# Optimization experiments

Measured on AMD Instinct MI355X. Metric: run time of the kernel, lower is better.

## Reference

```python
import jax, jax.numpy as jnp
import numpy as np

TAU = 1.0
BASE = 7
NUM_TWISTS = 3
EPS = 1e-6

B, S, D, P, M = 4, 2048, 1024, 9, 256


def _rot(y, theta):
    # learned rotation in the (0,1) channel plane; theta broadcasts against y[..., 0]
    c, s = jnp.cos(theta), jnp.sin(theta)
    y0, y1 = y[..., 0], y[..., 1]
    r0 = (y0 * c - y1 * s)[..., None]
    r1 = (y0 * s + y1 * c)[..., None]
    return jnp.concatenate([r0, r1, y[..., 2:]], axis=-1)


def _mod_phase_norm(x, g, base=BASE):
    # RMS-normalize within channel groups defined by (channel index mod base)
    d = x.shape[-1]
    gid = jnp.arange(d) % base
    oh = jax.nn.one_hot(gid, base, dtype=x.dtype)           # [d, base]
    cnt = oh.sum(axis=0)                                    # [base]
    msq = (x * x) @ oh / cnt                                # [..., base]
    denom = jnp.sqrt(jnp.take(msq, gid, axis=-1) + EPS)     # [..., d]
    return x / denom * g


def setup_inputs() -> dict:
    key = jax.random.key(0)
    ks = jax.random.split(key, 16)
    w = lambda k, shape, scale: jax.random.normal(k, shape, dtype=jnp.float32) * scale
    u = jax.random.uniform(ks[1], (NUM_TWISTS + 1, B, S, P), dtype=jnp.float32,
                           minval=1e-6, maxval=1.0 - 1e-6)
    gumbel_noise = -jnp.log(-jnp.log(u))
    return {
        'x': w(ks[0], (B, S, D), 1.0),
        'gumbel_noise': gumbel_noise,
        'mixer_w': w(ks[2], (3, D), 0.5),
        'obs_W1': w(ks[3], (2 * D, M), (2 * D) ** -0.5),
        'obs_b1': jnp.zeros((M,), jnp.float32),
        'obs_th1': w(ks[4], (), 0.1),
        'obs_W2': w(ks[5], (M, P), M ** -0.5),
        'obs_b2': jnp.zeros((P,), jnp.float32),
        'obs_th2': w(ks[6], (), 0.1),
        'path_Wa': w(ks[7], (P, D, M), D ** -0.5),
        'path_ba': jnp.zeros((P, M), jnp.float32),
        'path_tha': w(ks[8], (P,), 0.1),
        'path_Wb': w(ks[9], (P, M, D), M ** -0.5),
        'path_bb': jnp.zeros((P, D), jnp.float32),
        'path_thb': w(ks[10], (P,), 0.1),
        'twist_W': w(ks[11], (D, D), D ** -0.5),
        'twist_b': jnp.zeros((D,), jnp.float32),
        'twist_th': w(ks[12], (), 0.1),
        'norm_g': jnp.ones((D,), jnp.float32),
    }


def reference(x, gumbel_noise, mixer_w, obs_W1, obs_b1, obs_th1, obs_W2, obs_b2,
              obs_th2, path_Wa, path_ba, path_tha, path_Wb, path_bb, path_thb,
              twist_W, twist_b, twist_th, norm_g):
    # neighbor mixer: per-channel 3-tap mix over sequence (zero-padded, non-causal)
    xp = jnp.pad(x, ((0, 0), (1, 1), (0, 0)))
    x_mixed = x * mixer_w[0] + xp[:, :-2] * mixer_w[1] + xp[:, 2:] * mixer_w[2]

    def observer_logits(collapsed):
        combined = jnp.concatenate([x_mixed, collapsed], axis=-1)      # [B,S,2D]
        h = jnp.tanh(_rot(combined @ obs_W1 + obs_b1, obs_th1))        # [B,S,M]
        return _rot(h @ obs_W2 + obs_b2, obs_th2)                      # [B,S,P]

    def path_outputs_fn(tin):
        h = _rot(jnp.einsum('bsd,pdm->bspm', tin, path_Wa) + path_ba, path_tha)
        return _rot(jnp.einsum('bspm,pmd->bspd', h, path_Wb) + path_bb, path_thb)

    collapsed = jnp.zeros_like(x_mixed)
    path_out = None
    for t in range(NUM_TWISTS):
        logits = observer_logits(collapsed)
        rw = jax.nn.softmax((logits + gumbel_noise[t]) / TAU, axis=-1)  # soft gumbel
        tin = x_mixed + _rot(collapsed @ twist_W + twist_b, twist_th)
        path_out = path_outputs_fn(tin)                                # [B,S,P,D]
        collapsed = _mod_phase_norm(jnp.einsum('bspd,bsp->bsd', path_out, rw), norm_g)

    # final hard (straight-through) gumbel routing, reusing last path_out
    final_logits = observer_logits(collapsed)
    soft = jax.nn.softmax((final_logits + gumbel_noise[NUM_TWISTS]) / TAU, axis=-1)
    hard = jax.nn.one_hot(jnp.argmax(soft, axis=-1), P, dtype=soft.dtype)
    rw_hard = hard + soft - jax.lax.stop_gradient(soft)
    final_collapsed = jnp.einsum('bspd,bsp->bsd', path_out, rw_hard)

    # dropout is identity in eval mode
    out = _mod_phase_norm(x + final_collapsed, norm_g)
    collapsed = _mod_phase_norm(collapsed, norm_g)
    return out, collapsed
```

## Files before the change

### kernel.cpp

```cpp
#include <hip/hip_runtime.h>
#include <hip/hip_bf16.h>

typedef unsigned short u16;
typedef short bf16x8 __attribute__((ext_vector_type(8)));
typedef float f32x4 __attribute__((ext_vector_type(4)));

constexpr int Dd = 1024, Pp = 9, Mm = 256, Nn = 8192, Kc = 2304;
constexpr float EPSf = 1e-6f;

__device__ __forceinline__ float bf2f(u16 u) {
    union { unsigned int u; float f; } v; v.u = ((unsigned int)u) << 16; return v.f;
}
__device__ __forceinline__ u16 f2bf(float f) {
    union { float f; unsigned int u; } v; v.f = f;
    unsigned int r = (v.u + 0x7FFFu + ((v.u >> 16) & 1u)) >> 16; return (u16)r;
}
__device__ __forceinline__ void split2(float v, u16& h, u16& l) {
    h = f2bf(v); l = f2bf(v - bf2f(h));
}
__device__ __forceinline__ void gld16(u16* lds, const u16* g) {
    __builtin_amdgcn_global_load_lds(
        (const __attribute__((address_space(1))) unsigned int*)g,
        (__attribute__((address_space(3))) unsigned int*)lds, 16, 0, 0);
}
// ... 18 lines not shown
}

__global__ void splitW1_k(const float* __restrict__ W1, const float* __restrict__ th,
                          u16* __restrict__ h, u16* __restrict__ l)
{
    int idx = blockIdx.x * 256 + threadIdx.x;
    if (idx >= 256 * 2048) return;
    int k = idx & 2047, n = idx >> 11;
    float v;
    if (n == 0)      v = W1[(long)k * 256 + 0] * cosf(th[0]) - W1[(long)k * 256 + 1] * sinf(th[0]);
    else if (n == 1) v = W1[(long)k * 256 + 0] * sinf(th[0]) + W1[(long)k * 256 + 1] * cosf(th[0]);
    else             v = W1[(long)k * 256 + n];
    u16 hh, ll; split2(v, hh, ll); h[idx] = hh; l[idx] = ll;
}

__global__ void splitTW_k(const float* __restrict__ tW, const float* __restrict__ th,
                          u16* __restrict__ h, u16* __restrict__ l)
{
    int idx = blockIdx.x * 256 + threadIdx.x;
    if (idx >= 1024 * 1024) return;
    int k = idx & 1023, n = idx >> 10;
    float v;
    if (n == 0)      v = tW[(long)k * 1024 + 0] * cosf(th[0]) - tW[(long)k * 1024 + 1] * sinf(th[0]);
    else if (n == 1) v = tW[(long)k * 1024 + 0] * sinf(th[0]) + tW[(long)k * 1024 + 1] * cosf(th[0]);
    else             v = tW[(long)k * 1024 + n];
    u16 hh, ll; split2(v, hh, ll); h[idx] = hh; l[idx] = ll;
}

__global__ void splitWa_k(const float* __restrict__ Wa, const float* __restrict__ tha,
                          u16* __restrict__ h, u16* __restrict__ l)
{
    int idx = blockIdx.x * 256 + threadIdx.x;
    if (idx >= Kc * 1024) return;
    int k = idx & 1023, n = idx >> 10;
    int p = n >> 8, m = n & 255;
    const float* s = Wa + ((long)p * 1024 + k) * 256;
    float v;
    if (m == 0)      v = s[0] * cosf(tha[p]) - s[1] * sinf(tha[p]);
    else if (m == 1) v = s[0] * sinf(tha[p]) + s[1] * cosf(tha[p]);
    else             v = s[m];
// ... 2 lines not shown

__global__ void splitWb_k(const float* __restrict__ Wb, const float* __restrict__ thb,
                          u16* __restrict__ h, u16* __restrict__ l)
{
    int idx = blockIdx.x * 256 + threadIdx.x;
    if (idx >= 1024 * Kc) return;
    int n = idx / Kc;
    int k = idx - n * Kc;
    int p = k >> 8, m = k & 255;
    const float* s = Wb + ((long)p * 256 + m) * 1024;
    float v;
    if (n == 0)      v = s[0] * cosf(thb[p]) - s[1] * sinf(thb[p]);
    else if (n == 1) v = s[0] * sinf(thb[p]) + s[1] * cosf(thb[p]);
    else             v = s[n];
    u16 hh, ll; split2(v, hh, ll); h[idx] = hh; l[idx] = ll;
}

__global__ void mixer_k(const float* __restrict__ x, const float* __restrict__ mw,
                        u16* __restrict__ xmh, u16* __restrict__ xml)
{
    int idx = blockIdx.x * 256 + threadIdx.x;
    if (idx >= Nn * Dd / 4) return;
    int d4 = idx & (Dd / 4 - 1);
    int n = idx >> 8;
    int s = n & 2047;
    const float4* x4 = (const float4*)x;
    const float4* w4 = (const float4*)mw;
    float4 xc = x4[idx];
    float4 w0 = w4[d4], w1 = w4[(Dd / 4) + d4], w2 = w4[2 * (Dd / 4) + d4];
    float o[4];
// ... 6 lines not shown
        float4 xr = x4[idx + Dd / 4];
        o[0] += xr.x * w2.x; o[1] += xr.y * w2.y; o[2] += xr.z * w2.z; o[3] += xr.w * w2.w;
    }
    ushort4 h4, l4;
    split2(o[0], h4.x, l4.x); split2(o[1], h4.y, l4.y);
    split2(o[2], h4.z, l4.z); split2(o[3], h4.w, l4.w);
    ((ushort4*)xmh)[idx] = h4; ((ushort4*)xml)[idx] = l4;
}

__global__ void tanh_k(const float* __restrict__ a, float* __restrict__ o, int total)
{
    int idx = blockIdx.x * 256 + threadIdx.x;
    if (idx < total) o[idx] = tanhf(a[idx]);
}

__global__ void addb_split_k(const u16* __restrict__ xmh, const u16* __restrict__ xml,
                             const float* __restrict__ tbr,
                             u16* __restrict__ th_, u16* __restrict__ tl_)
{
    int idx = blockIdx.x * 256 + threadIdx.x;
    if (idx >= Nn * Dd / 4) return;
    int d4 = idx & (Dd / 4 - 1);
    ushort4 xh = ((const ushort4*)xmh)[idx], xl = ((const ushort4*)xml)[idx];
    float4 b = ((const float4*)tbr)[d4];
    ushort4 h4, l4;
    split2(bf2f(xh.x) + bf2f(xl.x) + b.x, h4.x, l4.x);
    split2(bf2f(xh.y) + bf2f(xl.y) + b.y, h4.y, l4.y);
    split2(bf2f(xh.z) + bf2f(xl.z) + b.z, h4.z, l4.z);
    split2(bf2f(xh.w) + bf2f(xl.w) + b.w, h4.w, l4.w);
    ((ushort4*)th_)[idx] = h4; ((ushort4*)tl_)[idx] = l4;
}

template<int EPI>
__global__ __launch_bounds__(256, 2) void mgemm(
    const u16* __restrict__ Agh, const u16* __restrict__ Agl, int lda,
    const u16* __restrict__ Bgh, const u16* __restrict__ Bgl, int ldb,
    int K,
    float* __restrict__ Cf, int ldc,
    const float* __restrict__ Cinit,
    const float* __restrict__ bias,
    const float* __restrict__ rwv,
    const float* __restrict__ rwv2,
    const float* __restrict__ bbrv)
{
    __shared__ u16 smem[2][16384];
    const int tid = threadIdx.x, wave = tid >> 6, lane = tid & 63;
    const int nwg = gridDim.x * gridDim.y;
    const int flat = blockIdx.y * gridDim.x + blockIdx.x;
    const int q = nwg >> 3;
    const int l_ = (flat & 7) * q + (flat >> 3);
    const int r0 = (l_ / gridDim.x) * 128, c0 = (l_ % gridDim.x) * 128;
    const int srl = lane >> 2;
    const int ssl = ((lane & 3) ^ ((lane >> 3) & 3)) * 8;
    const int frl = lane & 15, kh = lane >> 4;
    const int sw  = (kh ^ ((frl >> 1) & 3)) * 8;
    const int arow0 = (wave >> 1) * 64, bcol0 = (wave & 1) * 64;
    const int w32 = wave * 32;

    f32x4 acc[4][4] = {};
    f32x4 acc2[4][4];
    if constexpr (EPI == 4) {
#pragma unroll
        for (int i = 0; i < 4; ++i)
#pragma unroll
            for (int j = 0; j < 4; ++j) acc2[i][j] = f32x4{0.f, 0.f, 0.f, 0.f};
    }

    auto STAGE = [&](int buf, int k0) {
        u16* base = &smem[buf][0];
        u16* As_h = base;        u16* As_l = base + 4096;
        u16* Bs_h = base + 8192; u16* Bs_l = base + 12288;
        const long ga0 = (long)(r0 + w32 + srl) * lda + k0 + ssl;
        gld16(&As_h[w32 * 32],        Agh + ga0);
        gld16(&As_h[(w32 + 16) * 32], Agh + ga0 + 16L * lda);
        gld16(&As_l[w32 * 32],        Agl + ga0);
        gld16(&As_l[(w32 + 16) * 32], Agl + ga0 + 16L * lda);
        const long gb0 = (long)(c0 + w32 + srl) * ldb + k0 + ssl;
        gld16(&Bs_h[w32 * 32],        Bgh + gb0);
        gld16(&Bs_h[(w32 + 16) * 32], Bgh + gb0 + 16L * ldb);
        gld16(&Bs_l[w32 * 32],        Bgl + gb0);
        gld16(&Bs_l[(w32 + 16) * 32], Bgl + gb0 + 16L * ldb);
    };
    auto COMPUTE = [&](int buf, f32x4 (&ac)[4][4]) {
        u16* base = &smem[buf][0];
        u16* As_h = base;        u16* As_l = base + 4096;
        u16* Bs_h = base + 8192; u16* Bs_l = base + 12288;
        bf16x8 ah[4], al[4];
#pragma unroll
        for (int f = 0; f < 4; ++f) {
            int ao = (arow0 + f * 16 + frl) * 32 + sw;
            ah[f] = *(const bf16x8*)&As_h[ao];
            al[f] = *(const bf16x8*)&As_l[ao];
        }
#pragma unroll
        for (int j = 0; j < 4; ++j) {
            int bo = (bcol0 + j * 16 + frl) * 32 + sw;
            bf16x8 bh = *(const bf16x8*)&Bs_h[bo];
            bf16x8 bl = *(const bf16x8*)&Bs_l[bo];
#pragma unroll
            for (int i = 0; i < 4; ++i) {
                ac[i][j] = __builtin_amdgcn_mfma_f32_16x16x32_bf16(ah[i], bh, ac[i][j], 0, 0, 0);
                ac[i][j] = __builtin_amdgcn_mfma_f32_16x16x32_bf16(ah[i], bl, ac[i][j], 0, 0, 0);
                ac[i][j] = __builtin_amdgcn_mfma_f32_16x16x32_bf16(al[i], bh, ac[i][j], 0, 0, 0);
            }
        }
    };
    auto FLUSH = [&](int p) {
#pragma unroll
        for (int i = 0; i < 4; ++i)
#pragma unroll
            for (int reg = 0; reg < 4; ++reg) {
                float w = rwv[(long)(r0 + arow0 + i * 16 + kh * 4 + reg) * 9 + p];
#pragma unroll
                for (int j = 0; j < 4; ++j) {
                    acc[i][j][reg] += w * acc2[i][j][reg];
                    acc2[i][j][reg] = 0.f;
                }
            }
    };

    const int NT = K / 32;
    STAGE(0, 0);
#pragma unroll 1
    for (int t = 0; t < NT; t += 2) {
        STAGE(1, (t + 1) * 32);
        asm volatile("s_waitcnt vmcnt(8)" ::: "memory");
        __builtin_amdgcn_sched_barrier(0);
        __builtin_amdgcn_s_barrier();
        __builtin_amdgcn_sched_barrier(0);
        if constexpr (EPI == 4) COMPUTE(0, acc2); else COMPUTE(0, acc);
        __builtin_amdgcn_sched_barrier(0);
        __builtin_amdgcn_s_barrier();
        __builtin_amdgcn_sched_barrier(0);
        if (t + 2 < NT) {
            STAGE(0, (t + 2) * 32);
            asm volatile("s_waitcnt vmcnt(8)" ::: "memory");
        } else {
            asm volatile("s_waitcnt vmcnt(0)" ::: "memory");
        }
        __builtin_amdgcn_sched_barrier(0);
        __builtin_amdgcn_s_barrier();
        __builtin_amdgcn_sched_barrier(0);
        if constexpr (EPI == 4) COMPUTE(1, acc2); else COMPUTE(1, acc);
        __builtin_amdgcn_sched_barrier(0);
        __builtin_amdgcn_s_barrier();
        __builtin_amdgcn_sched_barrier(0);
        if constexpr (EPI == 4) {
            if (((t + 1) & 7) == 7) FLUSH((t + 1) >> 3);
        }
    }

#pragma unroll
    for (int i = 0; i < 4; ++i)
#pragma unroll
        for (int reg = 0; reg < 4; ++reg) {
            const int r = r0 + arow0 + i * 16 + kh * 4 + reg;
#pragma unroll
            for (int j = 0; j < 4; ++j) {
                const int c = c0 + bcol0 + j * 16 + frl;
                float v = acc[i][j][reg];
                if constexpr (EPI == 0) {
                    Cf[(long)r * ldc + c] = v + bias[c];
                } else if constexpr (EPI == 1) {
                    Cf[(long)r * ldc + c] = tanhf(v + Cinit[(long)r * ldc + c]);
                } else if constexpr (EPI == 4) {
#pragma unroll
                    for (int p = 0; p < 9; ++p) v += rwv2[(long)r * 9 + p] * bbrv[p * 1024 + c];
                    Cf[(long)r * ldc + c] = v;
                }
            }
        }
}

template<int EPI>
__global__ __launch_bounds__(512, 2) void mgemm3(
    const u16* __restrict__ Agh, const u16* __restrict__ Agl, int lda,
    const u16* __restrict__ Bgh, const u16* __restrict__ Bgl, int ldb,
    int K,
    float* __restrict__ Cf, u16* __restrict__ Coh, u16* __restrict__ Col, int ldc,
    const u16* __restrict__ CIh, const u16* __restrict__ CIl,
    const float* __restrict__ bias,
    const float* __restrict__ rwv,
    const float* __restrict__ bbrv)
{
    __shared__ u16 smem[2][24576];
    const int tid = threadIdx.x, wave = tid >> 6, lane = tid & 63;
    const int nwg = gridDim.x * gridDim.y;
    const int flat = blockIdx.y * gridDim.x + blockIdx.x;
    const int q = nwg >> 3;
    const int l_ = (flat & 7) * q + (flat >> 3);
    const int r0 = (l_ / gridDim.x) * 256, c0 = (l_ % gridDim.x) * 128;
    const int srl = lane >> 2;
    const int ssl = ((lane & 3) ^ ((lane >> 3) & 3)) * 8;
    const int frl = lane & 15, kh = lane >> 4;
    const int sw  = (kh ^ ((frl >> 1) & 3)) * 8;
    const int arow0 = (wave >> 1) * 64, bcol0 = (wave & 1) * 64;
    const int w32 = wave * 32, w16 = wave * 16;
    const int NT = K / 32;

    f32x4 acc[4][4] = {};

    auto STAGE = [&](int buf, int k0) {
        u16* Ash = &smem[buf][0];
        u16* Asl = &smem[buf][8192];
        u16* Bsh = &smem[buf][16384];
        u16* Bsl = &smem[buf][20480];
        const long ga = (long)(r0 + w32 + srl) * lda + k0 + ssl;
        gld16(&Ash[w32 * 32],        Agh + ga);
        gld16(&Ash[(w32 + 16) * 32], Agh + ga + 16L * lda);
        gld16(&Asl[w32 * 32],        Agl + ga);
        gld16(&Asl[(w32 + 16) * 32], Agl + ga + 16L * lda);
        const long gb = (long)(c0 + w16 + srl) * ldb + k0 + ssl;
        gld16(&Bsh[w16 * 32], Bgh + gb);
        gld16(&Bsl[w16 * 32], Bgl + gb);
    };
    auto COMPUTE = [&](int buf) {
        const u16* Ash = &smem[buf][0];
        const u16* Asl = &smem[buf][8192];
        const u16* Bsh = &smem[buf][16384];
        const u16* Bsl = &smem[buf][20480];
        bf16x8 ah[4], al[4], bh[4], bl[4];
#pragma unroll
        for (int f = 0; f < 4; ++f) {
            int ao = (arow0 + f * 16 + frl) * 32 + sw;
            ah[f] = *(const bf16x8*)&Ash[ao];
            al[f] = *(const bf16x8*)&Asl[ao];
            int bo = (bcol0 + f * 16 + frl) * 32 + sw;
            bh[f] = *(const bf16x8*)&Bsh[bo];
            bl[f] = *(const bf16x8*)&Bsl[bo];
        }
        __builtin_amdgcn_s_setprio(1);
#pragma unroll
        for (int j = 0; j < 4; ++j)
#pragma unroll
            for (int i = 0; i < 4; ++i) {
                acc[i][j] = __builtin_amdgcn_mfma_f32_16x16x32_bf16(ah[i], bh[j], acc[i][j], 0, 0, 0);
                acc[i][j] = __builtin_amdgcn_mfma_f32_16x16x32_bf16(ah[i], bl[j], acc[i][j], 0, 0, 0);
                acc[i][j] = __builtin_amdgcn_mfma_f32_16x16x32_bf16(al[i], bh[j], acc[i][j], 0, 0, 0);
            }
        __builtin_amdgcn_s_setprio(0);
    };

    STAGE(0, 0);
    asm volatile("s_waitcnt vmcnt(0)" ::: "memory");
    __builtin_amdgcn_sched_barrier(0);
    __builtin_amdgcn_s_barrier();
    __builtin_amdgcn_sched_barrier(0);

#pragma unroll 1
    for (int t = 0; t < NT; t += 2) {
        STAGE(1, (t + 1) * 32);
        COMPUTE(0);
        asm volatile("s_waitcnt vmcnt(0)" ::: "memory");
        __builtin_amdgcn_sched_barrier(0);
        __builtin_amdgcn_s_barrier();
        __builtin_amdgcn_sched_barrier(0);
        if (t + 2 < NT) STAGE(0, (t + 2) * 32);
        COMPUTE(1);
        asm volatile("s_waitcnt vmcnt(0)" ::: "memory");
        __builtin_amdgcn_sched_barrier(0);
        __builtin_amdgcn_s_barrier();
        __builtin_amdgcn_sched_barrier(0);
    }

#pragma unroll
    for (int i = 0; i < 4; ++i)
#pragma unroll
        for (int reg = 0; reg < 4; ++reg) {
            const int r = r0 + arow0 + i * 16 + kh * 4 + reg;
#pragma unroll
            for (int j = 0; j < 4; ++j) {
                const int c = c0 + bcol0 + j * 16 + frl;
                float v = acc[i][j][reg];
                if constexpr (EPI == 2) {
                    long o = (long)r * ldc + c;
                    v += bf2f(CIh[o]) + bf2f(CIl[o]) + bias[c];
                    u16 h, l; split2(v, h, l); Coh[o] = h; Col[o] = l;
                } else if constexpr (EPI == 3) {
                    long o = (long)r * ldc + c;
                    v = (v + bias[c]) * rwv[(long)r * 9 + (c >> 8)];
                    u16 h, l; split2(v, h, l); Coh[o] = h; Col[o] = l;
                } else {
#pragma unroll
                    for (int p = 0; p < 9; ++p) v += rwv[(long)r * 9 + p] * bbrv[p * 1024 + c];
                    Cf[(long)r * ldc + c] = v;
                }
            }
        }
}

__global__ void logits_k(const float* __restrict__ h, const float* __restrict__ W2r,
                         const float* __restrict__ b2r, const float* __restrict__ gum,
                         float* __restrict__ rwA, float* __restrict__ rwH,
                         const float* __restrict__ rwS, int hard)
{
    __shared__ float hs[Mm];
    __shared__ float lg[16];
    int n = blockIdx.x;
    for (int i = threadIdx.x; i < Mm; i += 64) hs[i] = h[(long)n * Mm + i];
    __syncthreads();
    if (threadIdx.x < Pp) {
        int p = threadIdx.x;
        float acc = b2r[p];
        for (int m = 0; m < Mm; ++m) acc += hs[m] * W2r[m * Pp + p];
        lg[p] = acc + gum[(long)n * Pp + p];
    }
    __syncthreads();
    if (threadIdx.x == 0) {
        float mx = lg[0]; int am = 0;
#pragma unroll
        for (int p = 1; p < Pp; ++p) if (lg[p] > mx) { mx = lg[p]; am = p; }
        if (hard) {
#pragma unroll
            for (int p = 0; p < Pp; ++p) {
                rwA[(long)n * Pp + p] = (p == am) ? 1.f / rwS[(long)n * Pp + p] : 0.f;
                rwH[(long)n * Pp + p] = (p == am) ? 1.f : 0.f;
            }
        } else {
            float e[Pp]; float ssum = 0.f;
#pragma unroll
            for (int p = 0; p < Pp; ++p) { e[p] = expf(lg[p] - mx); ssum += e[p]; }
#pragma unroll
            for (int p = 0; p < Pp; ++p) rwA[(long)n * Pp + p] = e[p] / ssum;
        }
    }
}

template<int INSPLIT, int OUTSPLIT>
__global__ void norm_k(const float* __restrict__ in,
                       const u16* __restrict__ inh, const u16* __restrict__ inl,
                       const float* __restrict__ add, const float* __restrict__ g,
                       float* __restrict__ outf, u16* __restrict__ oh, u16* __restrict__ ol)
// ... 26 lines not shown
        const float cnt = (t < 2) ? 147.f : 146.f;
        dn[t] = 1.f / sqrtf(sb[0][t] / cnt + EPSf);
    }
    __syncthreads();
#pragma unroll
    for (int i = 0; i < 4; ++i) {
        int d = t + i * 256;
        long o = (long)n * Dd + d;
        float ov = v[i] * dn[d % 7] * g[d];
        if (OUTSPLIT) { u16 h, l; split2(ov, h, l); oh[o] = h; ol[o] = l; }
        else outf[o] = ov;
    }
}

static inline int cdiv(long a, long b) { return (int)((a + b - 1) / b); }

extern "C" void kernel_launch(void* const* d_in, const int* in_sizes, int n_in,
                              void* d_out, int out_size, void* d_ws, size_t ws_size,
                              hipStream_t stream)
{
    const float* x    = (const float*)d_in[0];
    const float* gum  = (const float*)d_in[1];
    const float* mw   = (const float*)d_in[2];
    const float* W1   = (const float*)d_in[3];
    const float* b1   = (const float*)d_in[4];
    const float* th1  = (const float*)d_in[5];
    const float* W2   = (const float*)d_in[6];
    const float* b2   = (const float*)d_in[7];
    const float* th2  = (const float*)d_in[8];
    const float* Wa   = (const float*)d_in[9];
    const float* ba   = (const float*)d_in[10];
    const float* tha  = (const float*)d_in[11];
    const float* Wb   = (const float*)d_in[12];
    const float* bbv  = (const float*)d_in[13];
    const float* thb  = (const float*)d_in[14];
    const float* tW   = (const float*)d_in[15];
    const float* tb   = (const float*)d_in[16];
    const float* tth  = (const float*)d_in[17];
    const float* gnorm = (const float*)d_in[18];

    char* cur = (char*)d_ws;
    auto alloc = [&](size_t bytes) -> void* {
        void* r = (void*)cur; cur += (bytes + 255) & ~(size_t)255; return r;
    };
    void* region = alloc((size_t)Nn * Dd * 4);
    float* craw = (float*)region;
    float* hbuf = (float*)region;
    u16*   tinh = (u16*)region;
    u16*   tinl = tinh + (size_t)Nn * Dd;
    float* zx   = (float*)alloc((size_t)Nn * Mm * 4);
    float* rwS  = (float*)alloc((size_t)Nn * Pp * 4);
    float* rwD  = (float*)alloc((size_t)Nn * Pp * 4);
    float* rwH  = (float*)alloc((size_t)Nn * Pp * 4);
    u16* xmh  = (u16*)alloc((size_t)Nn * Dd * 2);
    u16* xml  = (u16*)alloc((size_t)Nn * Dd * 2);
    u16* colh = (u16*)alloc((size_t)Nn * Dd * 2);
    u16* coll = (u16*)alloc((size_t)Nn * Dd * 2);
    u16* hph  = (u16*)alloc((size_t)Nn * Kc * 2);
    u16* hpl  = (u16*)alloc((size_t)Nn * Kc * 2);
    u16* W1th = (u16*)alloc(256 * 2048 * 2);
    u16* W1tl = (u16*)alloc(256 * 2048 * 2);
    u16* tWth = (u16*)alloc(1024 * 1024 * 2);
    u16* tWtl = (u16*)alloc(1024 * 1024 * 2);
    u16* Wath = (u16*)alloc((size_t)Kc * 1024 * 2);
    u16* Watl = (u16*)alloc((size_t)Kc * 1024 * 2);
    u16* Wbth = (u16*)alloc((size_t)1024 * Kc * 2);
    u16* Wbtl = (u16*)alloc((size_t)1024 * Kc * 2);
    float* W2r = (float*)alloc(256 * 9 * 4);
    float* b1r = (float*)alloc(256 * 4);
    float* b2r = (float*)alloc(16 * 4);
    float* bac = (float*)alloc(Kc * 4);
    float* bbr = (float*)alloc(Pp * 1024 * 4);
    float* tbr = (float*)alloc(1024 * 4);
    if ((size_t)(cur - (char*)d_ws) > ws_size) return;

    float* out0 = (float*)d_out;
    float* out1 = out0 + (long)Nn * Dd;

    splitW1_k<<<2048, 256, 0, stream>>>(W1, th1, W1th, W1tl);
    splitTW_k<<<4096, 256, 0, stream>>>(tW, tth, tWth, tWtl);
    splitWa_k<<<cdiv((long)Kc * 1024, 256), 256, 0, stream>>>(Wa, tha, Wath, Watl);
    splitWb_k<<<cdiv((long)1024 * Kc, 256), 256, 0, stream>>>(Wb, thb, Wbth, Wbtl);
    rotcopy_k<<<cdiv(256L * 9, 256), 256, 0, stream>>>(W2, W2r, 256, 9, th2, 1);
    rotcopy_k<<<1, 256, 0, stream>>>(b1, b1r, 1, 256, th1, 1);
    rotcopy_k<<<1, 256, 0, stream>>>(b2, b2r, 1, 9, th2, 1);
    rotcopy_k<<<cdiv((long)Pp * Mm, 256), 256, 0, stream>>>(ba, bac, 1, 256, tha, 9);
    rotcopy_k<<<cdiv((long)Pp * 1024, 256), 256, 0, stream>>>(bbv, bbr, 1, 1024, thb, 9);
    rotcopy_k<<<cdiv(1024L, 256), 256, 0, stream>>>(tb, tbr, 1, 1024, tth, 1);

    mixer_k<<<Nn * Dd / 4 / 256, 256, 0, stream>>>(x, mw, xmh, xml);

    mgemm<0><<<dim3(2, 64), 256, 0, stream>>>(
        xmh, xml, 1024, W1th, W1tl, 2048, 1024,
        zx, 256, nullptr, b1r, nullptr, nullptr, nullptr);

    for (int t = 0; t < 3; ++t) {
        if (t == 0) {
            tanh_k<<<cdiv((long)Nn * Mm, 256), 256, 0, stream>>>(zx, hbuf, Nn * Mm);
        } else {
            mgemm<1><<<dim3(2, 64), 256, 0, stream>>>(
                colh, coll, 1024, W1th + 1024, W1tl + 1024, 2048, 1024,
                hbuf, 256, zx, nullptr, nullptr, nullptr, nullptr);
        }
        logits_k<<<Nn, 64, 0, stream>>>(hbuf, W2r, b2r, gum + (long)t * Nn * Pp,
                                        rwS, nullptr, nullptr, 0);
        if (t == 0) {
            addb_split_k<<<Nn * Dd / 4 / 256, 256, 0, stream>>>(xmh, xml, tbr, tinh, tinl);
        } else {
            mgemm3<2><<<dim3(8, 32), 512, 0, stream>>>(
                colh, coll, 1024, tWth, tWtl, 1024, 1024,
                nullptr, tinh, tinl, 1024, xmh, xml, tbr, nullptr, nullptr);
        }
        mgemm3<3><<<dim3(18, 32), 512, 0, stream>>>(
            tinh, tinl, 1024, Wath, Watl, 1024, 1024,
            nullptr, hph, hpl, Kc, nullptr, nullptr, bac, rwS, nullptr);
        mgemm3<5><<<dim3(8, 32), 512, 0, stream>>>(
            hph, hpl, Kc, Wbth, Wbtl, Kc, Kc,
            craw, nullptr, nullptr, 1024, nullptr, nullptr, nullptr, rwS, bbr);
        norm_k<0, 1><<<Nn, 256, 0, stream>>>(craw, nullptr, nullptr, nullptr, gnorm,
                                             nullptr, colh, coll);
    }

    mgemm<1><<<dim3(2, 64), 256, 0, stream>>>(
        colh, coll, 1024, W1th + 1024, W1tl + 1024, 2048, 1024,
        hbuf, 256, zx, nullptr, nullptr, nullptr, nullptr);
    logits_k<<<Nn, 64, 0, stream>>>(hbuf, W2r, b2r, gum + 3L * Nn * Pp,
                                    rwD, rwH, rwS, 1);
    mgemm<4><<<dim3(8, 64), 256, 0, stream>>>(
        hph, hpl, Kc, Wbth, Wbtl, Kc, Kc,
        craw, 1024, nullptr, nullptr, rwD, rwH, bbr);
    norm_k<0, 0><<<Nn, 256, 0, stream>>>(craw, nullptr, nullptr, x, gnorm, out0, nullptr, nullptr);
    norm_k<1, 0><<<Nn, 256, 0, stream>>>(nullptr, colh, coll, nullptr, gnorm, out1, nullptr, nullptr);
}
```

Baseline: 1.415 ms.

## Fold twist GEMM into path weights and bucket final hard routing by path

Precomputes the product of the path-A weights and the transposed twist matrix, plus a combined bias. The twist GEMM then folds into the path-A GEMM, and x_mixed·Wa is computed once and reused as an additive init across iterations. The final straight-through routing stores only the argmax index, buckets tokens per path, and runs the Wb GEMM for each token's chosen path only, instead of all nine. Narrow observer GEMMs move to a smaller 64-row tile kernel. Costs are an extra Nn×Kc split buffer, a changed rounding order from pre-multiplied weights, and a fixed per-path capacity (CAP) in the bucket step.

```diff
diff --git a/kernel.cpp b/kernel.cpp
--- a/kernel.cpp
+++ b/kernel.cpp
@@ -6,6 +6,7 @@
 typedef float f32x4 __attribute__((ext_vector_type(4)));
 
 constexpr int Dd = 1024, Pp = 9, Mm = 256, Nn = 8192, Kc = 2304;
+constexpr int CAP = 4096;
 constexpr float EPSf = 1e-6f;
 
 __device__ __forceinline__ float bf2f(u16 u) {
@@ -56,16 +57,17 @@
     u16 hh, ll; split2(v, hh, ll); h[idx] = hh; l[idx] = ll;
 }
 
-__global__ void splitTW_k(const float* __restrict__ tW, const float* __restrict__ th,
-                          u16* __restrict__ h, u16* __restrict__ l)
+__global__ void splitTWT_k(const float* __restrict__ tW, const float* __restrict__ th,
+                           u16* __restrict__ h, u16* __restrict__ l)
 {
     int idx = blockIdx.x * 256 + threadIdx.x;
     if (idx >= 1024 * 1024) return;
-    int k = idx & 1023, n = idx >> 10;
+    int d = idx & 1023, e = idx >> 10;
+    const float* s = tW + (long)e * 1024;
     float v;
-    if (n == 0)      v = tW[(long)k * 1024 + 0] * cosf(th[0]) - tW[(long)k * 1024 + 1] * sinf(th[0]);
-    else if (n == 1) v = tW[(long)k * 1024 + 0] * sinf(th[0]) + tW[(long)k * 1024 + 1] * cosf(th[0]);
-    else             v = tW[(long)k * 1024 + n];
+    if (d == 0)      v = s[0] * cosf(th[0]) - s[1] * sinf(th[0]);
+    else if (d == 1) v = s[0] * sinf(th[0]) + s[1] * cosf(th[0]);
+    else             v = s[d];
     u16 hh, ll; split2(v, hh, ll); h[idx] = hh; l[idx] = ll;
 }
 
@@ -98,6 +100,44 @@
     else if (n == 1) v = s[0] * sinf(thb[p]) + s[1] * cosf(thb[p]);
     else             v = s[n];
     u16 hh, ll; split2(v, hh, ll); h[idx] = hh; l[idx] = ll;
+}
+
+__global__ void bac2_k(const float* __restrict__ bac, const float* __restrict__ tbr,
+                       const u16* __restrict__ Wath, const u16* __restrict__ Watl,
+                       float* __restrict__ bac2)
+{
+    __shared__ float sb[256];
+    int pm = blockIdx.x;
+    int t = threadIdx.x;
+    float s = 0.f;
+    for (int d = t; d < 1024; d += 256) {
+        long o = (long)pm * 1024 + d;
+        s += tbr[d] * (bf2f(Wath[o]) + bf2f(Watl[o]));
+    }
+    sb[t] = s; __syncthreads();
+    for (int st = 128; st >= 1; st >>= 1) {
+        if (t < st) sb[t] += sb[t + st];
+        __syncthreads();
+    }
+    if (t == 0) bac2[pm] = bac[pm] + sb[0];
+}
+
+__global__ void hp0_k(const u16* __restrict__ zxah, const u16* __restrict__ zxal,
+                      const float* __restrict__ rw,
+                      u16* __restrict__ hph, u16* __restrict__ hpl)
+{
+    int idx = blockIdx.x * 256 + threadIdx.x;
+    if (idx >= Nn * Kc / 4) return;
+    int c4 = idx % (Kc / 4);
+    int n  = idx / (Kc / 4);
+    float w = rw[(long)n * Pp + (c4 >> 6)];
+    ushort4 zh = ((const ushort4*)zxah)[idx], zl = ((const ushort4*)zxal)[idx];
+    ushort4 h4, l4;
+    split2((bf2f(zh.x) + bf2f(zl.x)) * w, h4.x, l4.x);
+    split2((bf2f(zh.y) + bf2f(zl.y)) * w, h4.y, l4.y);
+    split2((bf2f(zh.z) + bf2f(zl.z)) * w, h4.z, l4.z);
+    split2((bf2f(zh.w) + bf2f(zl.w)) * w, h4.w, l4.w);
+    ((ushort4*)hph)[idx] = h4; ((ushort4*)hpl)[idx] = l4;
 }
 
 __global__ void mixer_k(const float* __restrict__ x, const float* __restrict__ mw,
@@ -134,33 +174,15 @@
     if (idx < total) o[idx] = tanhf(a[idx]);
 }
 
-__global__ void addb_split_k(const u16* __restrict__ xmh, const u16* __restrict__ xml,
-                             const float* __restrict__ tbr,
-                             u16* __restrict__ th_, u16* __restrict__ tl_)
-{
-    int idx = blockIdx.x * 256 + threadIdx.x;
-    if (idx >= Nn * Dd / 4) return;
-    int d4 = idx & (Dd / 4 - 1);
-    ushort4 xh = ((const ushort4*)xmh)[idx], xl = ((const ushort4*)xml)[idx];
-    float4 b = ((const float4*)tbr)[d4];
-    ushort4 h4, l4;
-    split2(bf2f(xh.x) + bf2f(xl.x) + b.x, h4.x, l4.x);
-    split2(bf2f(xh.y) + bf2f(xl.y) + b.y, h4.y, l4.y);
-    split2(bf2f(xh.z) + bf2f(xl.z) + b.z, h4.z, l4.z);
-    split2(bf2f(xh.w) + bf2f(xl.w) + b.w, h4.w, l4.w);
-    ((ushort4*)th_)[idx] = h4; ((ushort4*)tl_)[idx] = l4;
-}
-
 template<int EPI>
 __global__ __launch_bounds__(256, 2) void mgemm(
     const u16* __restrict__ Agh, const u16* __restrict__ Agl, int lda,
     const u16* __restrict__ Bgh, const u16* __restrict__ Bgl, int ldb,
     int K,
-    float* __restrict__ Cf, int ldc,
-    const float* __restrict__ Cinit,
+    float* __restrict__ Cf, u16* __restrict__ Coh, u16* __restrict__ Col, int ldc,
+    const u16* __restrict__ CIh, const u16* __restrict__ CIl,
     const float* __restrict__ bias,
     const float* __restrict__ rwv,
-    const float* __restrict__ rwv2,
     const float* __restrict__ bbrv)
 {
     __shared__ u16 smem[2][16384];
@@ -178,13 +200,6 @@
     const int w32 = wave * 32;
 
     f32x4 acc[4][4] = {};
-    f32x4 acc2[4][4];
-    if constexpr (EPI == 4) {
-#pragma unroll
-        for (int i = 0; i < 4; ++i)
-#pragma unroll
-            for (int j = 0; j < 4; ++j) acc2[i][j] = f32x4{0.f, 0.f, 0.f, 0.f};
-    }
 
     auto STAGE = [&](int buf, int k0) {
         u16* base = &smem[buf][0];
@@ -201,7 +216,7 @@
         gld16(&Bs_l[w32 * 32],        Bgl + gb0);
         gld16(&Bs_l[(w32 + 16) * 32], Bgl + gb0 + 16L * ldb);
     };
-    auto COMPUTE = [&](int buf, f32x4 (&ac)[4][4]) {
+    auto COMPUTE = [&](int buf) {
         u16* base = &smem[buf][0];
         u16* As_h = base;        u16* As_l = base + 4096;
         u16* Bs_h = base + 8192; u16* Bs_l = base + 12288;
@@ -219,24 +234,11 @@
             bf16x8 bl = *(const bf16x8*)&Bs_l[bo];
 #pragma unroll
             for (int i = 0; i < 4; ++i) {
-                ac[i][j] = __builtin_amdgcn_mfma_f32_16x16x32_bf16(ah[i], bh, ac[i][j], 0, 0, 0);
-                ac[i][j] = __builtin_amdgcn_mfma_f32_16x16x32_bf16(ah[i], bl, ac[i][j], 0, 0, 0);
-                ac[i][j] = __builtin_amdgcn_mfma_f32_16x16x32_bf16(al[i], bh, ac[i][j], 0, 0, 0);
+                acc[i][j] = __builtin_amdgcn_mfma_f32_16x16x32_bf16(ah[i], bh, acc[i][j], 0, 0, 0);
+                acc[i][j] = __builtin_amdgcn_mfma_f32_16x16x32_bf16(ah[i], bl, acc[i][j], 0, 0, 0);
+                acc[i][j] = __builtin_amdgcn_mfma_f32_16x16x32_bf16(al[i], bh, acc[i][j], 0, 0, 0);
             }
         }
-    };
-    auto FLUSH = [&](int p) {
-#pragma unroll
-        for (int i = 0; i < 4; ++i)
-#pragma unroll
-            for (int reg = 0; reg < 4; ++reg) {
-                float w = rwv[(long)(r0 + arow0 + i * 16 + kh * 4 + reg) * 9 + p];
-#pragma unroll
-                for (int j = 0; j < 4; ++j) {
-                    acc[i][j][reg] += w * acc2[i][j][reg];
-                    acc2[i][j][reg] = 0.f;
-                }
-            }
     };
 
     const int NT = K / 32;
@@ -248,7 +250,7 @@
         __builtin_amdgcn_sched_barrier(0);
         __builtin_amdgcn_s_barrier();
         __builtin_amdgcn_sched_barrier(0);
-        if constexpr (EPI == 4) COMPUTE(0, acc2); else COMPUTE(0, acc);
+        COMPUTE(0);
         __builtin_amdgcn_sched_barrier(0);
         __builtin_amdgcn_s_barrier();
         __builtin_amdgcn_sched_barrier(0);
@@ -261,13 +263,10 @@
         __builtin_amdgcn_sched_barrier(0);
         __builtin_amdgcn_s_barrier();
         __builtin_amdgcn_sched_barrier(0);
-        if constexpr (EPI == 4) COMPUTE(1, acc2); else COMPUTE(1, acc);
-        __builtin_amdgcn_sched_barrier(0);
-        __builtin_amdgcn_s_barrier();
-        __builtin_amdgcn_sched_barrier(0);
-        if constexpr (EPI == 4) {
-            if (((t + 1) & 7) == 7) FLUSH((t + 1) >> 3);
-        }
+        COMPUTE(1);
+        __builtin_amdgcn_sched_barrier(0);
+        __builtin_amdgcn_s_barrier();
+        __builtin_amdgcn_sched_barrier(0);
     }
 
 #pragma unroll
@@ -278,106 +277,236 @@
 #pragma unroll
             for (int j = 0; j < 4; ++j) {
                 const int c = c0 + bcol0 + j * 16 + frl;
+                const long o = (long)r * ldc + c;
                 float v = acc[i][j][reg];
-                if constexpr (EPI == 0) {
-                    Cf[(long)r * ldc + c] = v + bias[c];
-                } else if constexpr (EPI == 1) {
-                    Cf[(long)r * ldc + c] = tanhf(v + Cinit[(long)r * ldc + c]);
-                } else if constexpr (EPI == 4) {
-#pragma unroll
-                    for (int p = 0; p < 9; ++p) v += rwv2[(long)r * 9 + p] * bbrv[p * 1024 + c];
-                    Cf[(long)r * ldc + c] = v;
+                if constexpr (EPI == 5) {
+#pragma unroll
+                    for (int p = 0; p < 9; ++p) v += rwv[(long)r * 9 + p] * bbrv[p * 1024 + c];
+                    Cf[o] = v;
+                } else if constexpr (EPI == 6) {
+                    if (bias) v += bias[c];
+                    u16 h, l; split2(v, h, l); Coh[o] = h; Col[o] = l;
+                } else {
+                    v = (v + bf2f(CIh[o]) + bf2f(CIl[o])) * rwv[(long)r * 9 + (c >> 8)];
+                    u16 h, l; split2(v, h, l); Coh[o] = h; Col[o] = l;
                 }
             }
         }
 }
 
 template<int EPI>
-__global__ __launch_bounds__(512, 2) void mgemm3(
+__global__ __launch_bounds__(128, 2) void mgemmS(
     const u16* __restrict__ Agh, const u16* __restrict__ Agl, int lda,
     const u16* __restrict__ Bgh, const u16* __restrict__ Bgl, int ldb,
     int K,
-    float* __restrict__ Cf, u16* __restrict__ Coh, u16* __restrict__ Col, int ldc,
-    const u16* __restrict__ CIh, const u16* __restrict__ CIl,
-    const float* __restrict__ bias,
-    const float* __restrict__ rwv,
-    const float* __restrict__ bbrv)
-{
-    __shared__ u16 smem[2][24576];
+    float* __restrict__ Cf, int ldc,
+    const float* __restrict__ Cinit,
+    const float* __restrict__ bias)
+{
+    __shared__ u16 smem[2][12288];
     const int tid = threadIdx.x, wave = tid >> 6, lane = tid & 63;
     const int nwg = gridDim.x * gridDim.y;
     const int flat = blockIdx.y * gridDim.x + blockIdx.x;
     const int q = nwg >> 3;
     const int l_ = (flat & 7) * q + (flat >> 3);
-    const int r0 = (l_ / gridDim.x) * 256, c0 = (l_ % gridDim.x) * 128;
+    const int r0 = (l_ / gridDim.x) * 64, c0 = (l_ % gridDim.x) * 128;
+    const int srl = lane >> 2;
+    const int ssl = ((lane & 3) ^ ((lane >> 3) & 3)) * 8;
+    const int frl = lane & 15, kh = lane >> 4;
+    const int sw  = (kh ^ ((frl >> 1) & 3)) * 8;
+    const int w32 = wave * 32, w64 = wave * 64;
+
+    f32x4 acc[4][4] = {};
+
+    auto STAGE = [&](int buf, int k0) {
+        u16* Ash = &smem[buf][0];
+        u16* Asl = &smem[buf][2048];
+        u16* Bsh = &smem[buf][4096];
+        u16* Bsl = &smem[buf][8192];
+        const long ga = (long)(r0 + w32 + srl) * lda + k0 + ssl;
+        gld16(&Ash[w32 * 32],        Agh + ga);
+        gld16(&Ash[(w32 + 16) * 32], Agh + ga + 16L * lda);
+        gld16(&Asl[w32 * 32],        Agl + ga);
+        gld16(&Asl[(w32 + 16) * 32], Agl + ga + 16L * lda);
+        const long gb = (long)(c0 + w64 + srl) * ldb + k0 + ssl;
+        gld16(&Bsh[w64 * 32],        Bgh + gb);
+        gld16(&Bsh[(w64 + 16) * 32], Bgh + gb + 16L * ldb);
+        gld16(&Bsh[(w64 + 32) * 32], Bgh + gb + 32L * ldb);
+        gld16(&Bsh[(w64 + 48) * 32], Bgh + gb + 48L * ldb);
+        gld16(&Bsl[w64 * 32],        Bgl + gb);
+        gld16(&Bsl[(w64 + 16) * 32], Bgl + gb + 16L * ldb);
+        gld16(&Bsl[(w64 + 32) * 32], Bgl + gb + 32L * ldb);
+        gld16(&Bsl[(w64 + 48) * 32], Bgl + gb + 48L * ldb);
+    };
+    auto COMPUTE = [&](int buf) {
+        u16* Ash = &smem[buf][0];
+        u16* Asl = &smem[buf][2048];
+        u16* Bsh = &smem[buf][4096];
+        u16* Bsl = &smem[buf][8192];
+        bf16x8 ah[4], al[4];
+#pragma unroll
+        for (int f = 0; f < 4; ++f) {
+            int ao = (f * 16 + frl) * 32 + sw;
+            ah[f] = *(const bf16x8*)&Ash[ao];
+            al[f] = *(const bf16x8*)&Asl[ao];
+        }
+#pragma unroll
+        for (int j = 0; j < 4; ++j) {
+            int bo = (w64 + j * 16 + frl) * 32 + sw;
+            bf16x8 bh = *(const bf16x8*)&Bsh[bo];
+            bf16x8 bl = *(const bf16x8*)&Bsl[bo];
+#pragma unroll
+            for (int i = 0; i < 4; ++i) {
+                acc[i][j] = __builtin_amdgcn_mfma_f32_16x16x32_bf16(ah[i], bh, acc[i][j], 0, 0, 0);
+                acc[i][j] = __builtin_amdgcn_mfma_f32_16x16x32_bf16(ah[i], bl, acc[i][j], 0, 0, 0);
+                acc[i][j] = __builtin_amdgcn_mfma_f32_16x16x32_bf16(al[i], bh, acc[i][j], 0, 0, 0);
+            }
+        }
+    };
+
+    const int NT = K / 32;
+    STAGE(0, 0);
+#pragma unroll 1
+    for (int t = 0; t < NT; t += 2) {
+        STAGE(1, (t + 1) * 32);
+        asm volatile("s_waitcnt vmcnt(12)" ::: "memory");
+        __builtin_amdgcn_sched_barrier(0);
+        __builtin_amdgcn_s_barrier();
+        __builtin_amdgcn_sched_barrier(0);
+        COMPUTE(0);
+        __builtin_amdgcn_sched_barrier(0);
+        __builtin_amdgcn_s_barrier();
+        __builtin_amdgcn_sched_barrier(0);
+        if (t + 2 < NT) {
+            STAGE(0, (t + 2) * 32);
+            asm volatile("s_waitcnt vmcnt(12)" ::: "memory");
+        } else {
+            asm volatile("s_waitcnt vmcnt(0)" ::: "memory");
+        }
+        __builtin_amdgcn_sched_barrier(0);
+        __builtin_amdgcn_s_barrier();
+        __builtin_amdgcn_sched_barrier(0);
+        COMPUTE(1);
+        __builtin_amdgcn_sched_barrier(0);
+        __builtin_amdgcn_s_barrier();
+        __builtin_amdgcn_sched_barrier(0);
+    }
+
+#pragma unroll
+    for (int i = 0; i < 4; ++i)
+#pragma unroll
+        for (int reg = 0; reg < 4; ++reg) {
+            const int r = r0 + i * 16 + kh * 4 + reg;
+#pragma unroll
+            for (int j = 0; j < 4; ++j) {
+                const int c = c0 + w64 + j * 16 + frl;
+                const long o = (long)r * ldc + c;
+                float v = acc[i][j][reg];
+                if constexpr (EPI == 0) Cf[o] = v + bias[c];
+                else                    Cf[o] = tanhf(v + Cinit[o]);
+            }
+        }
+}
+
+__global__ void bucket_k(const int* __restrict__ pstar, int* __restrict__ cnt,
+                         int* __restrict__ perm)
+{
+    int n = blockIdx.x * 256 + threadIdx.x;
+    if (n >= Nn) return;
+    int p = pstar[n];
+    int slot = atomicAdd(&cnt[p], 1);
+    if (slot < CAP) perm[p * CAP + slot] = n;
+}
+
+__global__ __launch_bounds__(256, 2) void mgemm_fin(
+    const u16* __restrict__ hph, const u16* __restrict__ hpl,
+    const u16* __restrict__ Wbth, const u16* __restrict__ Wbtl,
+    const int* __restrict__ perm, const int* __restrict__ cnt,
+    const float* __restrict__ rwS, const float* __restrict__ bbr,
+    float* __restrict__ craw)
+{
+    __shared__ u16 smem[2][16384];
+    const int tid = threadIdx.x, wave = tid >> 6, lane = tid & 63;
+    const int p = blockIdx.y >> 5;
+    const int rb0 = (blockIdx.y & 31) * 128;
+    const int cntp = cnt[p];
+    if (rb0 >= cntp) return;
+    const int c0 = blockIdx.x * 128;
+    const int pbase = p * 256;
     const int srl = lane >> 2;
     const int ssl = ((lane & 3) ^ ((lane >> 3) & 3)) * 8;
     const int frl = lane & 15, kh = lane >> 4;
     const int sw  = (kh ^ ((frl >> 1) & 3)) * 8;
     const int arow0 = (wave >> 1) * 64, bcol0 = (wave & 1) * 64;
-    const int w32 = wave * 32, w16 = wave * 16;
-    const int NT = K / 32;
+    const int w32 = wave * 32;
+    const int tok0 = perm[p * CAP + rb0 + w32 + srl];
+    const int tok1 = perm[p * CAP + rb0 + w32 + 16 + srl];
 
     f32x4 acc[4][4] = {};
 
     auto STAGE = [&](int buf, int k0) {
-        u16* Ash = &smem[buf][0];
-        u16* Asl = &smem[buf][8192];
-        u16* Bsh = &smem[buf][16384];
-        u16* Bsl = &smem[buf][20480];
-        const long ga = (long)(r0 + w32 + srl) * lda + k0 + ssl;
-        gld16(&Ash[w32 * 32],        Agh + ga);
-        gld16(&Ash[(w32 + 16) * 32], Agh + ga + 16L * lda);
-        gld16(&Asl[w32 * 32],        Agl + ga);
-        gld16(&Asl[(w32 + 16) * 32], Agl + ga + 16L * lda);
-        const long gb = (long)(c0 + w16 + srl) * ldb + k0 + ssl;
-        gld16(&Bsh[w16 * 32], Bgh + gb);
-        gld16(&Bsl[w16 * 32], Bgl + gb);
+        u16* base = &smem[buf][0];
+        u16* As_h = base;        u16* As_l = base + 4096;
+        u16* Bs_h = base + 8192; u16* Bs_l = base + 12288;
+        const long ga0 = (long)tok0 * Kc + pbase + k0 + ssl;
+        const long ga1 = (long)tok1 * Kc + pbase + k0 + ssl;
+        gld16(&As_h[w32 * 32],        hph + ga0);
+        gld16(&As_h[(w32 + 16) * 32], hph + ga1);
+        gld16(&As_l[w32 * 32],        hpl + ga0);
+        gld16(&As_l[(w32 + 16) * 32], hpl + ga1);
+        const long gb0 = (long)(c0 + w32 + srl) * Kc + pbase + k0 + ssl;
+        gld16(&Bs_h[w32 * 32],        Wbth + gb0);
+        gld16(&Bs_h[(w32 + 16) * 32], Wbth + gb0 + 16L * Kc);
+        gld16(&Bs_l[w32 * 32],        Wbtl + gb0);
+        gld16(&Bs_l[(w32 + 16) * 32], Wbtl + gb0 + 16L * Kc);
     };
     auto COMPUTE = [&](int buf) {
-        const u16* Ash = &smem[buf][0];
-        const u16* Asl = &smem[buf][8192];
-        const u16* Bsh = &smem[buf][16384];
-        const u16* Bsl = &smem[buf][20480];
-        bf16x8 ah[4], al[4], bh[4], bl[4];
+        u16* base = &smem[buf][0];
+        u16* As_h = base;        u16* As_l = base + 4096;
+        u16* Bs_h = base + 8192; u16* Bs_l = base + 12288;
+        bf16x8 ah[4], al[4];
 #pragma unroll
         for (int f = 0; f < 4; ++f) {
             int ao = (arow0 + f * 16 + frl) * 32 + sw;
-            ah[f] = *(const bf16x8*)&Ash[ao];
-            al[f] = *(const bf16x8*)&Asl[ao];
-            int bo = (bcol0 + f * 16 + frl) * 32 + sw;
-            bh[f] = *(const bf16x8*)&Bsh[bo];
-            bl[f] = *(const bf16x8*)&Bsl[bo];
-        }
-        __builtin_amdgcn_s_setprio(1);
-#pragma unroll
-        for (int j = 0; j < 4; ++j)
+            ah[f] = *(const bf16x8*)&As_h[ao];
+            al[f] = *(const bf16x8*)&As_l[ao];
+        }
+#pragma unroll
+        for (int j = 0; j < 4; ++j) {
+            int bo = (bcol0 + j * 16 + frl) * 32 + sw;
+            bf16x8 bh = *(const bf16x8*)&Bs_h[bo];
+            bf16x8 bl = *(const bf16x8*)&Bs_l[bo];
 #pragma unroll
             for (int i = 0; i < 4; ++i) {
-                acc[i][j] = __builtin_amdgcn_mfma_f32_16x16x32_bf16(ah[i], bh[j], acc[i][j], 0, 0, 0);
-                acc[i][j] = __builtin_amdgcn_mfma_f32_16x16x32_bf16(ah[i], bl[j], acc[i][j], 0, 0, 0);
-                acc[i][j] = __builtin_amdgcn_mfma_f32_16x16x32_bf16(al[i], bh[j], acc[i][j], 0, 0, 0);
+                acc[i][j] = __builtin_amdgcn_mfma_f32_16x16x32_bf16(ah[i], bh, acc[i][j], 0, 0, 0);
+                acc[i][j] = __builtin_amdgcn_mfma_f32_16x16x32_bf16(ah[i], bl, acc[i][j], 0, 0, 0);
+                acc[i][j] = __builtin_amdgcn_mfma_f32_16x16x32_bf16(al[i], bh, acc[i][j], 0, 0, 0);
             }
-        __builtin_amdgcn_s_setprio(0);
+        }
     };
 
     STAGE(0, 0);
-    asm volatile("s_waitcnt vmcnt(0)" ::: "memory");
-    __builtin_amdgcn_sched_barrier(0);
-    __builtin_amdgcn_s_barrier();
-    __builtin_amdgcn_sched_barrier(0);
-
 #pragma unroll 1
-    for (int t = 0; t < NT; t += 2) {
+    for (int t = 0; t < 8; t += 2) {
         STAGE(1, (t + 1) * 32);
+        asm volatile("s_waitcnt vmcnt(8)" ::: "memory");
+        __builtin_amdgcn_sched_barrier(0);
+        __builtin_amdgcn_s_barrier();
+        __builtin_amdgcn_sched_barrier(0);
         COMPUTE(0);
-        asm volatile("s_waitcnt vmcnt(0)" ::: "memory");
-        __builtin_amdgcn_sched_barrier(0);
-        __builtin_amdgcn_s_barrier();
-        __builtin_amdgcn_sched_barrier(0);
-        if (t + 2 < NT) STAGE(0, (t + 2) * 32);
+        __builtin_amdgcn_sched_barrier(0);
+        __builtin_amdgcn_s_barrier();
+        __builtin_amdgcn_sched_barrier(0);
+        if (t + 2 < 8) {
+            STAGE(0, (t + 2) * 32);
+            asm volatile("s_waitcnt vmcnt(8)" ::: "memory");
+        } else {
+            asm volatile("s_waitcnt vmcnt(0)" ::: "memory");
+        }
+        __builtin_amdgcn_sched_barrier(0);
+        __builtin_amdgcn_s_barrier();
+        __builtin_amdgcn_sched_barrier(0);
         COMPUTE(1);
-        asm volatile("s_waitcnt vmcnt(0)" ::: "memory");
         __builtin_amdgcn_sched_barrier(0);
         __builtin_amdgcn_s_barrier();
         __builtin_amdgcn_sched_barrier(0);
@@ -387,23 +516,14 @@
     for (int i = 0; i < 4; ++i)
 #pragma unroll
         for (int reg = 0; reg < 4; ++reg) {
-            const int r = r0 + arow0 + i * 16 + kh * 4 + reg;
-#pragma unroll
-            for (int j = 0; j < 4; ++j) {
-                const int c = c0 + bcol0 + j * 16 + frl;
-                float v = acc[i][j][reg];
-                if constexpr (EPI == 2) {
-                    long o = (long)r * ldc + c;
-                    v += bf2f(CIh[o]) + bf2f(CIl[o]) + bias[c];
-                    u16 h, l; split2(v, h, l); Coh[o] = h; Col[o] = l;
-                } else if constexpr (EPI == 3) {
-                    long o = (long)r * ldc + c;
-                    v = (v + bias[c]) * rwv[(long)r * 9 + (c >> 8)];
-                    u16 h, l; split2(v, h, l); Coh[o] = h; Col[o] = l;
-                } else {
-#pragma unroll
-                    for (int p = 0; p < 9; ++p) v += rwv[(long)r * 9 + p] * bbrv[p * 1024 + c];
-                    Cf[(long)r * ldc + c] = v;
+            const int gr = rb0 + arow0 + i * 16 + kh * 4 + reg;
+            if (gr < cntp) {
+                const int tokr = perm[p * CAP + gr];
+                const float w = 1.f / rwS[(long)tokr * Pp + p];
+#pragma unroll
+                for (int j = 0; j < 4; ++j) {
+                    const int c = c0 + bcol0 + j * 16 + frl;
+                    craw[(long)tokr * Dd + c] = acc[i][j][reg] * w + bbr[p * 1024 + c];
                 }
             }
         }
@@ -411,8 +531,7 @@
 
 __global__ void logits_k(const float* __restrict__ h, const float* __restrict__ W2r,
                          const float* __restrict__ b2r, const float* __restrict__ gum,
-                         float* __restrict__ rwA, float* __restrict__ rwH,
-                         const float* __restrict__ rwS, int hard)
+                         float* __restrict__ rwA, int* __restrict__ pstar, int hard)
 {
     __shared__ float hs[Mm];
     __shared__ float lg[16];
@@ -431,11 +550,7 @@
 #pragma unroll
         for (int p = 1; p < Pp; ++p) if (lg[p] > mx) { mx = lg[p]; am = p; }
         if (hard) {
-#pragma unroll
-            for (int p = 0; p < Pp; ++p) {
-                rwA[(long)n * Pp + p] = (p == am) ? 1.f / rwS[(long)n * Pp + p] : 0.f;
-                rwH[(long)n * Pp + p] = (p == am) ? 1.f : 0.f;
-            }
+            pstar[n] = am;
         } else {
             float e[Pp]; float ssum = 0.f;
 #pragma unroll
@@ -492,6 +607,7 @@
 }
 
 static inline int cdiv(long a, long b) { return (int)((a + b - 1) / b); }
+static inline size_t al256(size_t b) { return (b + 255) & ~(size_t)255; }
 
 extern "C" void kernel_launch(void* const* d_in, const int* in_sizes, int n_in,
                               void* d_out, int out_size, void* d_ws, size_t ws_size,
@@ -518,45 +634,47 @@
     const float* gnorm = (const float*)d_in[18];
 
     char* cur = (char*)d_ws;
-    auto alloc = [&](size_t bytes) -> void* {
-        void* r = (void*)cur; cur += (bytes + 255) & ~(size_t)255; return r;
-    };
+    auto alloc = [&](size_t bytes) -> void* { void* r = cur; cur += al256(bytes); return r; };
+
     void* region = alloc((size_t)Nn * Dd * 4);
-    float* craw = (float*)region;
-    float* hbuf = (float*)region;
-    u16*   tinh = (u16*)region;
-    u16*   tinl = tinh + (size_t)Nn * Dd;
     float* zx   = (float*)alloc((size_t)Nn * Mm * 4);
     float* rwS  = (float*)alloc((size_t)Nn * Pp * 4);
-    float* rwD  = (float*)alloc((size_t)Nn * Pp * 4);
-    float* rwH  = (float*)alloc((size_t)Nn * Pp * 4);
-    u16* xmh  = (u16*)alloc((size_t)Nn * Dd * 2);
-    u16* xml  = (u16*)alloc((size_t)Nn * Dd * 2);
     u16* colh = (u16*)alloc((size_t)Nn * Dd * 2);
     u16* coll = (u16*)alloc((size_t)Nn * Dd * 2);
     u16* hph  = (u16*)alloc((size_t)Nn * Kc * 2);
     u16* hpl  = (u16*)alloc((size_t)Nn * Kc * 2);
     u16* W1th = (u16*)alloc(256 * 2048 * 2);
     u16* W1tl = (u16*)alloc(256 * 2048 * 2);
-    u16* tWth = (u16*)alloc(1024 * 1024 * 2);
-    u16* tWtl = (u16*)alloc(1024 * 1024 * 2);
     u16* Wath = (u16*)alloc((size_t)Kc * 1024 * 2);
     u16* Watl = (u16*)alloc((size_t)Kc * 1024 * 2);
     u16* Wbth = (u16*)alloc((size_t)1024 * Kc * 2);
     u16* Wbtl = (u16*)alloc((size_t)1024 * Kc * 2);
-    float* W2r = (float*)alloc(256 * 9 * 4);
-    float* b1r = (float*)alloc(256 * 4);
-    float* b2r = (float*)alloc(16 * 4);
-    float* bac = (float*)alloc(Kc * 4);
-    float* bbr = (float*)alloc(Pp * 1024 * 4);
-    float* tbr = (float*)alloc(1024 * 4);
+    u16* zxah  = (u16*)alloc((size_t)Nn * Kc * 2);
+    u16* zxal  = (u16*)alloc((size_t)Nn * Kc * 2);
+    u16* tWtTh = (u16*)alloc((size_t)1024 * 1024 * 2);
+    u16* tWtTl = (u16*)alloc((size_t)1024 * 1024 * 2);
+    u16* Wfath = (u16*)alloc((size_t)Kc * 1024 * 2);
+    u16* Wfatl = (u16*)alloc((size_t)Kc * 1024 * 2);
+    float* W2r  = (float*)alloc(256 * 9 * 4);
+    float* b1r  = (float*)alloc(256 * 4);
+    float* b2r  = (float*)alloc(64);
+    float* bac  = (float*)alloc(Kc * 4);
+    float* bac2 = (float*)alloc(Kc * 4);
+    float* bbr  = (float*)alloc(Pp * 1024 * 4);
+    float* tbr  = (float*)alloc(1024 * 4);
+    int* pstar = (int*)alloc(Nn * 4);
+    int* perm  = (int*)alloc((size_t)Pp * CAP * 4);
+    int* cnt   = (int*)alloc(Pp * 4);
     if ((size_t)(cur - (char*)d_ws) > ws_size) return;
 
+    float* hbuf = (float*)region;
+    float* craw = (float*)region;
+    u16* xmh = (u16*)region;
+    u16* xml = xmh + (size_t)Nn * Dd;
     float* out0 = (float*)d_out;
     float* out1 = out0 + (long)Nn * Dd;
 
     splitW1_k<<<2048, 256, 0, stream>>>(W1, th1, W1th, W1tl);
-    splitTW_k<<<4096, 256, 0, stream>>>(tW, tth, tWth, tWtl);
     splitWa_k<<<cdiv((long)Kc * 1024, 256), 256, 0, stream>>>(Wa, tha, Wath, Watl);
     splitWb_k<<<cdiv((long)1024 * Kc, 256), 256, 0, stream>>>(Wb, thb, Wbth, Wbtl);
     rotcopy_k<<<cdiv(256L * 9, 256), 256, 0, stream>>>(W2, W2r, 256, 9, th2, 1);
@@ -565,48 +683,54 @@
     rotcopy_k<<<cdiv((long)Pp * Mm, 256), 256, 0, stream>>>(ba, bac, 1, 256, tha, 9);
     rotcopy_k<<<cdiv((long)Pp * 1024, 256), 256, 0, stream>>>(bbv, bbr, 1, 1024, thb, 9);
     rotcopy_k<<<cdiv(1024L, 256), 256, 0, stream>>>(tb, tbr, 1, 1024, tth, 1);
+    splitTWT_k<<<4096, 256, 0, stream>>>(tW, tth, tWtTh, tWtTl);
+    hipMemsetAsync(perm, 0, (size_t)Pp * CAP * 4, stream);
+    hipMemsetAsync(cnt, 0, Pp * 4, stream);
+
+    mgemm<6><<<dim3(8, 18), 256, 0, stream>>>(
+        Wath, Watl, 1024, tWtTh, tWtTl, 1024, 1024,
+        nullptr, Wfath, Wfatl, 1024, nullptr, nullptr, nullptr, nullptr, nullptr);
+    bac2_k<<<Kc, 256, 0, stream>>>(bac, tbr, Wath, Watl, bac2);
 
     mixer_k<<<Nn * Dd / 4 / 256, 256, 0, stream>>>(x, mw, xmh, xml);
-
-    mgemm<0><<<dim3(2, 64), 256, 0, stream>>>(
-        xmh, xml, 1024, W1th, W1tl, 2048, 1024,
-        zx, 256, nullptr, b1r, nullptr, nullptr, nullptr);
+    mgemmS<0><<<dim3(2, 128), 128, 0, stream>>>(
+        xmh, xml, 1024, W1th, W1tl, 2048, 1024, zx, 256, nullptr, b1r);
+    mgemm<6><<<dim3(18, 64), 256, 0, stream>>>(
+        xmh, xml, 1024, Wath, Watl, 1024, 1024,
+        nullptr, zxah, zxal, Kc, nullptr, nullptr, bac2, nullptr, nullptr);
 
     for (int t = 0; t < 3; ++t) {
         if (t == 0) {
             tanh_k<<<cdiv((long)Nn * Mm, 256), 256, 0, stream>>>(zx, hbuf, Nn * Mm);
         } else {
-            mgemm<1><<<dim3(2, 64), 256, 0, stream>>>(
+            mgemmS<1><<<dim3(2, 128), 128, 0, stream>>>(
                 colh, coll, 1024, W1th + 1024, W1tl + 1024, 2048, 1024,
-                hbuf, 256, zx, nullptr, nullptr, nullptr, nullptr);
+                hbuf, 256, zx, nullptr);
         }
         logits_k<<<Nn, 64, 0, stream>>>(hbuf, W2r, b2r, gum + (long)t * Nn * Pp,
-                                        rwS, nullptr, nullptr, 0);
+                                        rwS, nullptr, 0);
         if (t == 0) {
-            addb_split_k<<<Nn * Dd / 4 / 256, 256, 0, stream>>>(xmh, xml, tbr, tinh, tinl);
+            hp0_k<<<cdiv((long)Nn * Kc / 4, 256), 256, 0, stream>>>(zxah, zxal, rwS, hph, hpl);
         } else {
-            mgemm3<2><<<dim3(8, 32), 512, 0, stream>>>(
-                colh, coll, 1024, tWth, tWtl, 1024, 1024,
-                nullptr, tinh, tinl, 1024, xmh, xml, tbr, nullptr, nullptr);
-        }
-        mgemm3<3><<<dim3(18, 32), 512, 0, stream>>>(
-            tinh, tinl, 1024, Wath, Watl, 1024, 1024,
-            nullptr, hph, hpl, Kc, nullptr, nullptr, bac, rwS, nullptr);
-        mgemm3<5><<<dim3(8, 32), 512, 0, stream>>>(
+            mgemm<7><<<dim3(18, 64), 256, 0, stream>>>(
+                colh, coll, 1024, Wfath, Wfatl, 1024, 1024,
+                nullptr, hph, hpl, Kc, zxah, zxal, nullptr, rwS, nullptr);
+        }
+        mgemm<5><<<dim3(8, 64), 256, 0, stream>>>(
             hph, hpl, Kc, Wbth, Wbtl, Kc, Kc,
             craw, nullptr, nullptr, 1024, nullptr, nullptr, nullptr, rwS, bbr);
         norm_k<0, 1><<<Nn, 256, 0, stream>>>(craw, nullptr, nullptr, nullptr, gnorm,
                                              nullptr, colh, coll);
     }
 
-    mgemm<1><<<dim3(2, 64), 256, 0, stream>>>(
+    mgemmS<1><<<dim3(2, 128), 128, 0, stream>>>(
         colh, coll, 1024, W1th + 1024, W1tl + 1024, 2048, 1024,
-        hbuf, 256, zx, nullptr, nullptr, nullptr, nullptr);
+        hbuf, 256, zx, nullptr);
     logits_k<<<Nn, 64, 0, stream>>>(hbuf, W2r, b2r, gum + 3L * Nn * Pp,
-                                    rwD, rwH, rwS, 1);
-    mgemm<4><<<dim3(8, 64), 256, 0, stream>>>(
-        hph, hpl, Kc, Wbth, Wbtl, Kc, Kc,
-        craw, 1024, nullptr, nullptr, rwD, rwH, bbr);
+                                    nullptr, pstar, 1);
+    bucket_k<<<32, 256, 0, stream>>>(pstar, cnt, perm);
+    mgemm_fin<<<dim3(8, Pp * 32), 256, 0, stream>>>(
+        hph, hpl, Wbth, Wbtl, perm, cnt, rwS, bbr, craw);
     norm_k<0, 0><<<Nn, 256, 0, stream>>>(craw, nullptr, nullptr, x, gnorm, out0, nullptr, nullptr);
     norm_k<1, 0><<<Nn, 256, 0, stream>>>(nullptr, colh, coll, nullptr, gnorm, out1, nullptr, nullptr);
 }
```

Result: faster. 1.333 ms (-5.9%).
